# Optimization experiments

Hardware: AMD Instinct MI355X
Metric: run time of the kernel (lower is better)

The kernel has to match this reference:

```python
import jax, jax.numpy as jnp
import numpy as np

L, B, S, D, W = 3, 32, 512, 512, 3
EPS = 1e-6

def setup_inputs() -> dict:
    key = jax.random.key(0)
    ks = jax.random.split(key, 12)
    s = 1.0 / np.sqrt(D)
    def n(k, shape, scale=1.0):
        return jax.random.normal(k, shape, dtype=jnp.float32) * scale
    return {
        'x': n(ks[0], (B, S, D)),
        'fwd_pad': n(ks[1], (L, W, D), s),
        'bwd_pad': n(ks[2], (L, W, D), s),
        'fwd_w': n(ks[3], (L, W + 1)),
        'bwd_w': n(ks[4], (L, W + 1)),
        'fwd_w1': n(ks[5], (L, D, D), s),
        'fwd_b1': jnp.zeros((L, D), jnp.float32),
        'fwd_w2': n(ks[6], (L, D, D), s),
        'fwd_b2': jnp.zeros((L, D), jnp.float32),
        'fwd_g': jnp.ones((L, D), jnp.float32),
        'fwd_beta': jnp.zeros((L, D), jnp.float32),
        'bwd_w1': n(ks[7], (L, D, D), s),
        'bwd_b1': jnp.zeros((L, D), jnp.float32),
        'bwd_w2': n(ks[8], (L, D, D), s),
        'bwd_b2': jnp.zeros((L, D), jnp.float32),
        'bwd_g': jnp.ones((L, D), jnp.float32),
        'bwd_beta': jnp.zeros((L, D), jnp.float32),
    }

def _ln(y, g, b):
    # Annotated-transformer LayerNorm: a2*(x-mean)/(std+eps)+b2, unbiased std
    m = y.mean(-1, keepdims=True)
    sd = jnp.std(y, -1, keepdims=True, ddof=1)
    return g * (y - m) / (sd + EPS) + b

def _ffn(y, w1, b1, w2, b2):
    h = jax.nn.relu(jnp.einsum('bsd,de->bse', y, w1) + b1)
    return jnp.einsum('bse,ef->bsf', h, w2) + b2

def _wsum(padded, w, seq_len, offset):
    # weighted sum over a sliding window of width W+1 (dropout=0, eval mode)
    win = jnp.stack([padded[:, offset + k: offset + k + seq_len] for k in range(W + 1)], 0)
    return jnp.einsum('k,kbsd->bsd', w, win)

def reference(x, fwd_pad, bwd_pad, fwd_w, bwd_w,
              fwd_w1, fwd_b1, fwd_w2, fwd_b2, fwd_g, fwd_beta,
              bwd_w1, bwd_b1, bwd_w2, bwd_b2, bwd_g, bwd_beta):
    bsz, seq_len, _ = x.shape
    xf, xb = x, x
    outs = []
    for i in range(L):
        fp = jnp.broadcast_to(fwd_pad[i], (bsz, W, D))
        bp = jnp.broadcast_to(bwd_pad[i], (bsz, W, D))
        pf = jnp.concatenate([fp, xf, bp], axis=1)  # [B, S+2W, D]
        pb = jnp.concatenate([fp, xb, bp], axis=1)
        yf = _wsum(pf, fwd_w[i], seq_len, 0)       # windows [t, t+W]
        yb = _wsum(pb, bwd_w[i], seq_len, W)       # windows [t+W, t+2W]
        xf = yf + _ffn(_ln(yf, fwd_g[i], fwd_beta[i]), fwd_w1[i], fwd_b1[i], fwd_w2[i], fwd_b2[i])
        xb = yb + _ffn(_ln(yb, bwd_g[i], bwd_beta[i]), bwd_w1[i], bwd_b1[i], bwd_w2[i], bwd_b2[i])
        outs.append(jnp.concatenate([xf, xb], axis=-1))
    return jnp.stack(outs, 0)  # [L, B, S, 2D]
```

## Files before the change

kernel.cpp:

```cpp
#include <hip/hip_runtime.h>

#define S_LEN 512
#define D_DIM 512
#define BATCH 32
#define M_ROWS (BATCH * S_LEN)
#define NLAYER 3

typedef unsigned short ushort_t;
typedef __bf16 bf16_t;
typedef bf16_t bf16x8 __attribute__((ext_vector_type(8)));
typedef unsigned short u16x8 __attribute__((ext_vector_type(8)));
typedef float f32x4 __attribute__((ext_vector_type(4)));

typedef const __attribute__((address_space(1))) unsigned int* gptr_t;
typedef __attribute__((address_space(3))) unsigned int* lptr_t;

__device__ __forceinline__ ushort_t f2bf(float f) {
  unsigned u = __float_as_uint(f);
  unsigned r = (u + 0x7fffu + ((u >> 16) & 1u)) >> 16;
  return (ushort_t)r;
}

__global__ __launch_bounds__(256)
void wprep_kernel(const float* __restrict__ fw1, const float* __restrict__ fw2,
                  const float* __restrict__ bw1, const float* __restrict__ bw2,
                  ushort_t* __restrict__ wt1, ushort_t* __restrict__ wt2) {
  int z = blockIdx.z;
  int l = z >> 2, m = z & 3;
  const float* bases[4] = {fw1, fw2, bw1, bw2};
  const float* src = bases[m] + (size_t)l * D_DIM * D_DIM;
  int streamIdx = m >> 1;
  int which = m & 1;
  ushort_t* dst = (which ? wt2 : wt1) + ((size_t)streamIdx * NLAYER + l) * D_DIM * D_DIM;

  __shared__ float tile[32][33];
  int n0 = blockIdx.x * 32, k0 = blockIdx.y * 32;
  int tx = threadIdx.x, ty = threadIdx.y;
#pragma unroll
  for (int i = 0; i < 32; i += 8)
    tile[ty + i][tx] = src[(size_t)(k0 + ty + i) * D_DIM + n0 + tx];
  __syncthreads();
#pragma unroll
  for (int i = 0; i < 32; i += 8)
    dst[(size_t)(n0 + ty + i) * D_DIM + k0 + tx] = f2bf(tile[tx][ty + i]);
}

__global__ __launch_bounds__(256)
void conv_ln_kernel(const float* __restrict__ srcF, int strideF,
                    const float* __restrict__ srcB, int strideB,
                    const float* __restrict__ padLo, const float* __restrict__ padHi,
                    const float* __restrict__ wF, const float* __restrict__ wB,
                    const float* __restrict__ gF, const float* __restrict__ beF,
                    const float* __restrict__ gB, const float* __restrict__ beB,
                    ushort_t* __restrict__ yln) {
  int z = blockIdx.y;
  int tid = threadIdx.x;
  int lane = tid & 63;
  int rl = tid >> 6;
  int row = blockIdx.x * 4 + rl;
  int t = row & (S_LEN - 1);
  const float* src = z ? srcB : srcF;
  int stride = z ? strideB : strideF;
  const float* wv = z ? wB : wF;
  const float* gv = z ? gB : gF;
  const float* bv = z ? beB : beF;
  int toff = z ? 0 : -3;
  int c0 = lane * 4, c1 = 256 + lane * 4;

  float4 a0 = make_float4(0.f, 0.f, 0.f, 0.f);
  float4 a1 = make_float4(0.f, 0.f, 0.f, 0.f);
#pragma unroll
  for (int k = 0; k < 4; ++k) {
    int tt = t + k + toff;
    const float* rp;
    if (tt < 0)            rp = padLo + (size_t)(tt + 3) * D_DIM;
    else if (tt >= S_LEN)  rp = padHi + (size_t)(tt - S_LEN) * D_DIM;
    else                   rp = src + (size_t)(row + k + toff) * stride;
    float wk = wv[k];
    float4 u0 = *(const float4*)(rp + c0);
    float4 u1 = *(const float4*)(rp + c1);
    a0.x = fmaf(wk, u0.x, a0.x); a0.y = fmaf(wk, u0.y, a0.y);
    a0.z = fmaf(wk, u0.z, a0.z); a0.w = fmaf(wk, u0.w, a0.w);
    a1.x = fmaf(wk, u1.x, a1.x); a1.y = fmaf(wk, u1.y, a1.y);
    a1.z = fmaf(wk, u1.z, a1.z); a1.w = fmaf(wk, u1.w, a1.w);
  }
  float s = a0.x + a0.y + a0.z + a0.w + a1.x + a1.y + a1.z + a1.w;
#pragma unroll
  for (int o = 32; o; o >>= 1) s += __shfl_xor(s, o);
  float mean = s * (1.0f / 512.0f);
  float q = 0.f, dx;
  dx = a0.x - mean; q = fmaf(dx, dx, q);
  dx = a0.y - mean; q = fmaf(dx, dx, q);
  dx = a0.z - mean; q = fmaf(dx, dx, q);
  dx = a0.w - mean; q = fmaf(dx, dx, q);
  dx = a1.x - mean; q = fmaf(dx, dx, q);
  dx = a1.y - mean; q = fmaf(dx, dx, q);
  dx = a1.z - mean; q = fmaf(dx, dx, q);
  dx = a1.w - mean; q = fmaf(dx, dx, q);
#pragma unroll
  for (int o = 32; o; o >>= 1) q += __shfl_xor(q, o);
  float sd = sqrtf(q * (1.0f / 511.0f));
  float inv = 1.0f / (sd + 1e-6f);

  size_t base = ((size_t)z * M_ROWS + row) * D_DIM;
  float4 g0 = *(const float4*)(gv + c0), g1 = *(const float4*)(gv + c1);
  float4 b0 = *(const float4*)(bv + c0), b1 = *(const float4*)(bv + c1);
  ushort_t p0[4], p1[4];
  p0[0] = f2bf(g0.x * ((a0.x - mean) * inv) + b0.x);
  p0[1] = f2bf(g0.y * ((a0.y - mean) * inv) + b0.y);
  p0[2] = f2bf(g0.z * ((a0.z - mean) * inv) + b0.z);
  p0[3] = f2bf(g0.w * ((a0.w - mean) * inv) + b0.w);
  p1[0] = f2bf(g1.x * ((a1.x - mean) * inv) + b1.x);
  p1[1] = f2bf(g1.y * ((a1.y - mean) * inv) + b1.y);
  p1[2] = f2bf(g1.z * ((a1.z - mean) * inv) + b1.z);
  p1[3] = f2bf(g1.w * ((a1.w - mean) * inv) + b1.w);
  *(uint2*)(yln + base + c0) = *(uint2*)p0;
  *(uint2*)(yln + base + c1) = *(uint2*)p1;
}

template <int EPI>
__global__ __launch_bounds__(256)
void gemm_kernel(const ushort_t* __restrict__ A,
                 const ushort_t* __restrict__ Bt_f, const ushort_t* __restrict__ Bt_b,
                 const float* __restrict__ bias_f, const float* __restrict__ bias_b,
                 ushort_t* __restrict__ Hout,
                 float* __restrict__ Cout,
                 const float* __restrict__ srcF, const float* __restrict__ srcB,
                 int srcStride,
                 const float* __restrict__ padLo, const float* __restrict__ padHi,
                 const float* __restrict__ wF, const float* __restrict__ wB) {
  const int K = 512;
  int lin = blockIdx.x;
  int xcd = lin & 7;
  int slot = lin >> 3;
  int nblk = slot & 3;
  int G = xcd * 32 + (slot >> 2);
  int z = G >> 7;
  int mblk = G & 127;

  const ushort_t* Ab = A + (size_t)z * M_ROWS * K + (size_t)mblk * 128 * K;
  const ushort_t* Bb = (z ? Bt_b : Bt_f) + (size_t)nblk * 128 * K;

  __shared__ __attribute__((aligned(16))) ushort_t As[128 * 32];
  __shared__ __attribute__((aligned(16))) ushort_t Bs[128 * 32];

  int tid = threadIdx.x, lane = tid & 63, wave = tid >> 6;
  int wr = wave >> 1, wc = wave & 1;
  int lm = lane & 15, lq = lane >> 4;

  f32x4 acc[4][4] = {};

  for (int kb = 0; kb < 16; ++kb) {
    int k0 = kb * 32;
#pragma unroll
    for (int i = 0; i < 2; ++i) {
      int slot2 = i * 256 + tid;
      int row = slot2 >> 2, kc = slot2 & 3;
      const ushort_t* ga = Ab + (size_t)row * K + k0 + kc * 8;
      const ushort_t* gb = Bb + (size_t)row * K + k0 + kc * 8;
      __builtin_amdgcn_global_load_lds((gptr_t)(const void*)ga,
                                       (lptr_t)(void*)(As + slot2 * 8), 16, 0, 0);
      __builtin_amdgcn_global_load_lds((gptr_t)(const void*)gb,
                                       (lptr_t)(void*)(Bs + slot2 * 8), 16, 0, 0);
    }
    __syncthreads();
    bf16x8 a[4], b[4];
#pragma unroll
    for (int i = 0; i < 4; ++i) {
      union { u16x8 u; bf16x8 b; } ua, ub;
      ua.u = *(const u16x8*)&As[(wr * 64 + i * 16 + lm) * 32 + lq * 8];
      ub.u = *(const u16x8*)&Bs[(wc * 64 + i * 16 + lm) * 32 + lq * 8];
      a[i] = ua.b; b[i] = ub.b;
    }
#pragma unroll
    for (int i = 0; i < 4; ++i)
#pragma unroll
      for (int j = 0; j < 4; ++j)
        acc[i][j] = __builtin_amdgcn_mfma_f32_16x16x32_bf16(a[i], b[j], acc[i][j], 0, 0, 0);
    __syncthreads();
  }

  const float* bias = z ? bias_b : bias_f;
  if (EPI == 1) {
    ushort_t* Hb = Hout + (size_t)z * M_ROWS * 512;
#pragma unroll
    for (int i = 0; i < 4; ++i) {
      int mbase = mblk * 128 + wr * 64 + i * 16 + lq * 4;
#pragma unroll
      for (int j = 0; j < 4; ++j) {
        int n = nblk * 128 + wc * 64 + j * 16 + lm;
        float bvn = bias[n];
#pragma unroll
        for (int r = 0; r < 4; ++r) {
          float v = fmaxf(acc[i][j][r] + bvn, 0.0f);
          Hb[(size_t)(mbase + r) * 512 + n] = f2bf(v);
        }
      }
    }
  } else {
    const float* src = z ? srcB : srcF;
    const float* wv = z ? wB : wF;
    int toff = z ? 0 : -3;
    float w0 = wv[0], w1 = wv[1], w2 = wv[2], w3 = wv[3];
    float* Cb = Cout + (size_t)z * 512;
#pragma unroll
    for (int i = 0; i < 4; ++i) {
      int mbase = mblk * 128 + wr * 64 + i * 16 + lq * 4;
      int t0 = mbase & (S_LEN - 1);
      int rb = mbase - t0;
      const float* rp[7];
#pragma unroll
      for (int q = 0; q < 7; ++q) {
        int tt = t0 + toff + q;
        rp[q] = (tt < 0)       ? padLo + (size_t)(tt + 3) * D_DIM
              : (tt >= S_LEN)  ? padHi + (size_t)(tt - S_LEN) * D_DIM
                               : src + (size_t)(rb + tt) * srcStride;
      }
#pragma unroll
      for (int j = 0; j < 4; ++j) {
        int n = nblk * 128 + wc * 64 + j * 16 + lm;
        float v[7];
#pragma unroll
        for (int q = 0; q < 7; ++q) v[q] = rp[q][n];
        float bvn = bias[n];
#pragma unroll
        for (int r = 0; r < 4; ++r) {
          float y = w0 * v[r] + w1 * v[r + 1] + w2 * v[r + 2] + w3 * v[r + 3];
          Cb[(size_t)(mbase + r) * 1024 + n] = acc[i][j][r] + bvn + y;
        }
      }
    }
  }
}

extern "C" void kernel_launch(void* const* d_in, const int* in_sizes, int n_in,
                              void* d_out, int out_size, void* d_ws, size_t ws_size,
                              hipStream_t stream) {
  const float* x        = (const float*)d_in[0];
  const float* fwd_pad  = (const float*)d_in[1];
  const float* bwd_pad  = (const float*)d_in[2];
  const float* fwd_w    = (const float*)d_in[3];
  const float* bwd_w    = (const float*)d_in[4];
  const float* fwd_w1   = (const float*)d_in[5];
  const float* fwd_b1   = (const float*)d_in[6];
  const float* fwd_w2   = (const float*)d_in[7];
  const float* fwd_b2   = (const float*)d_in[8];
  const float* fwd_g    = (const float*)d_in[9];
  const float* fwd_beta = (const float*)d_in[10];
  const float* bwd_w1   = (const float*)d_in[11];
  const float* bwd_b1   = (const float*)d_in[12];
  const float* bwd_w2   = (const float*)d_in[13];
  const float* bwd_b2   = (const float*)d_in[14];
  const float* bwd_g    = (const float*)d_in[15];
  const float* bwd_beta = (const float*)d_in[16];
  float* out = (float*)d_out;

  const size_t WSZ = (size_t)D_DIM * D_DIM;
  ushort_t* wt1 = (ushort_t*)d_ws;
  ushort_t* wt2 = wt1 + 2 * NLAYER * WSZ;
  ushort_t* yln = wt2 + 2 * NLAYER * WSZ;
  ushort_t* h   = yln + (size_t)2 * M_ROWS * D_DIM;

  wprep_kernel<<<dim3(16, 16, 12), dim3(32, 8), 0, stream>>>(
      fwd_w1, fwd_w2, bwd_w1, bwd_w2, wt1, wt2);

  for (int l = 0; l < NLAYER; ++l) {
    const float *srcF, *srcB;
    int str;
    if (l == 0) {
      srcF = x; srcB = x; str = 512;
    } else {
      srcF = out + (size_t)(l - 1) * M_ROWS * 1024;
      srcB = srcF + 512;
      str = 1024;
    }
    const float* pLo = fwd_pad + (size_t)l * 3 * D_DIM;
    const float* pHi = bwd_pad + (size_t)l * 3 * D_DIM;

    conv_ln_kernel<<<dim3(M_ROWS / 4, 2), 256, 0, stream>>>(
        srcF, str, srcB, str, pLo, pHi,
        fwd_w + l * 4, bwd_w + l * 4,
        fwd_g + l * D_DIM, fwd_beta + l * D_DIM,
        bwd_g + l * D_DIM, bwd_beta + l * D_DIM,
        yln);

    gemm_kernel<1><<<1024, 256, 0, stream>>>(
        yln, wt1 + (size_t)l * WSZ, wt1 + (size_t)(NLAYER + l) * WSZ,
        fwd_b1 + l * D_DIM, bwd_b1 + l * D_DIM,
        h, nullptr,
        nullptr, nullptr, 0, nullptr, nullptr, nullptr, nullptr);

    gemm_kernel<2><<<1024, 256, 0, stream>>>(
        h, wt2 + (size_t)l * WSZ, wt2 + (size_t)(NLAYER + l) * WSZ,
        fwd_b2 + l * D_DIM, bwd_b2 + l * D_DIM,
        nullptr, out + (size_t)l * M_ROWS * 1024,
        srcF, srcB, str, pLo, pHi,
        fwd_w + l * 4, bwd_w + l * 4);
  }
}
```

Baseline: 513.4 us.

## Store bf16 conv output for residual, widen GEMM K-step, stage H stores through LDS

The conv/LN kernel now also writes the windowed-sum result y as bf16 to a workspace buffer. The second GEMM epilogue reads that residual directly instead of recomputing the 4-tap window from 7 fp32 rows. The GEMM main loop loads a 64-wide K slice per barrier pair, halving the number of syncs. The first GEMM epilogue stages the bf16 ReLU output in LDS so it can be written with coalesced 16-byte row stores. The residual is now rounded to bf16, which costs accuracy, and the extra write plus larger LDS footprint may reduce occupancy.

```diff
diff --git a/kernel.cpp b/kernel.cpp
--- a/kernel.cpp
+++ b/kernel.cpp
@@ -19,6 +19,9 @@
   unsigned u = __float_as_uint(f);
   unsigned r = (u + 0x7fffu + ((u >> 16) & 1u)) >> 16;
   return (ushort_t)r;
+}
+__device__ __forceinline__ float bf2f(ushort_t h) {
+  return __uint_as_float(((unsigned)h) << 16);
 }
 
 __global__ __launch_bounds__(256)
@@ -52,7 +55,7 @@
                     const float* __restrict__ wF, const float* __restrict__ wB,
                     const float* __restrict__ gF, const float* __restrict__ beF,
                     const float* __restrict__ gB, const float* __restrict__ beB,
-                    ushort_t* __restrict__ yln) {
+                    ushort_t* __restrict__ yln, ushort_t* __restrict__ yfb) {
   int z = blockIdx.y;
   int tid = threadIdx.x;
   int lane = tid & 63;
@@ -103,6 +106,13 @@
   float inv = 1.0f / (sd + 1e-6f);
 
   size_t base = ((size_t)z * M_ROWS + row) * D_DIM;
+
+  ushort_t f0[4], f1[4];
+  f0[0] = f2bf(a0.x); f0[1] = f2bf(a0.y); f0[2] = f2bf(a0.z); f0[3] = f2bf(a0.w);
+  f1[0] = f2bf(a1.x); f1[1] = f2bf(a1.y); f1[2] = f2bf(a1.z); f1[3] = f2bf(a1.w);
+  *(uint2*)(yfb + base + c0) = *(uint2*)f0;
+  *(uint2*)(yfb + base + c1) = *(uint2*)f1;
+
   float4 g0 = *(const float4*)(gv + c0), g1 = *(const float4*)(gv + c1);
   float4 b0 = *(const float4*)(bv + c0), b1 = *(const float4*)(bv + c1);
   ushort_t p0[4], p1[4];
@@ -118,6 +128,8 @@
   *(uint2*)(yln + base + c1) = *(uint2*)p1;
 }
 
+#define RPITCH 136
+
 template <int EPI>
 __global__ __launch_bounds__(256)
 void gemm_kernel(const ushort_t* __restrict__ A,
@@ -125,10 +137,7 @@
                  const float* __restrict__ bias_f, const float* __restrict__ bias_b,
                  ushort_t* __restrict__ Hout,
                  float* __restrict__ Cout,
-                 const float* __restrict__ srcF, const float* __restrict__ srcB,
-                 int srcStride,
-                 const float* __restrict__ padLo, const float* __restrict__ padHi,
-                 const float* __restrict__ wF, const float* __restrict__ wB) {
+                 const ushort_t* __restrict__ yfb) {
   const int K = 512;
   int lin = blockIdx.x;
   int xcd = lin & 7;
@@ -141,8 +150,9 @@
   const ushort_t* Ab = A + (size_t)z * M_ROWS * K + (size_t)mblk * 128 * K;
   const ushort_t* Bb = (z ? Bt_b : Bt_f) + (size_t)nblk * 128 * K;
 
-  __shared__ __attribute__((aligned(16))) ushort_t As[128 * 32];
-  __shared__ __attribute__((aligned(16))) ushort_t Bs[128 * 32];
+  __shared__ __attribute__((aligned(16))) ushort_t sm[128 * RPITCH];
+  ushort_t* As = sm;
+  ushort_t* Bs = sm + 8192;
 
   int tid = threadIdx.x, lane = tid & 63, wave = tid >> 6;
   int wr = wave >> 1, wc = wave & 1;
@@ -150,39 +160,66 @@
 
   f32x4 acc[4][4] = {};
 
-  for (int kb = 0; kb < 16; ++kb) {
-    int k0 = kb * 32;
-#pragma unroll
-    for (int i = 0; i < 2; ++i) {
-      int slot2 = i * 256 + tid;
-      int row = slot2 >> 2, kc = slot2 & 3;
-      const ushort_t* ga = Ab + (size_t)row * K + k0 + kc * 8;
-      const ushort_t* gb = Bb + (size_t)row * K + k0 + kc * 8;
+  for (int kb = 0; kb < 8; ++kb) {
+    int k0 = kb * 64;
+#pragma unroll
+    for (int i = 0; i < 4; ++i) {
+      int s2 = i * 256 + tid;
+      int half = s2 >> 9;
+      int rem = s2 & 511;
+      int row = rem >> 2, kc = rem & 3;
+      const ushort_t* ga = Ab + (size_t)row * K + k0 + half * 32 + kc * 8;
+      const ushort_t* gb = Bb + (size_t)row * K + k0 + half * 32 + kc * 8;
       __builtin_amdgcn_global_load_lds((gptr_t)(const void*)ga,
-                                       (lptr_t)(void*)(As + slot2 * 8), 16, 0, 0);
+                                       (lptr_t)(void*)(As + s2 * 8), 16, 0, 0);
       __builtin_amdgcn_global_load_lds((gptr_t)(const void*)gb,
-                                       (lptr_t)(void*)(Bs + slot2 * 8), 16, 0, 0);
+                                       (lptr_t)(void*)(Bs + s2 * 8), 16, 0, 0);
     }
     __syncthreads();
-    bf16x8 a[4], b[4];
-#pragma unroll
-    for (int i = 0; i < 4; ++i) {
-      union { u16x8 u; bf16x8 b; } ua, ub;
-      ua.u = *(const u16x8*)&As[(wr * 64 + i * 16 + lm) * 32 + lq * 8];
-      ub.u = *(const u16x8*)&Bs[(wc * 64 + i * 16 + lm) * 32 + lq * 8];
-      a[i] = ua.b; b[i] = ub.b;
-    }
-#pragma unroll
-    for (int i = 0; i < 4; ++i)
-#pragma unroll
-      for (int j = 0; j < 4; ++j)
-        acc[i][j] = __builtin_amdgcn_mfma_f32_16x16x32_bf16(a[i], b[j], acc[i][j], 0, 0, 0);
+#pragma unroll
+    for (int s = 0; s < 2; ++s) {
+      bf16x8 a[4], b[4];
+#pragma unroll
+      for (int i = 0; i < 4; ++i) {
+        union { u16x8 u; bf16x8 b; } ua, ub;
+        ua.u = *(const u16x8*)&As[s * 4096 + (wr * 64 + i * 16 + lm) * 32 + lq * 8];
+        ub.u = *(const u16x8*)&Bs[s * 4096 + (wc * 64 + i * 16 + lm) * 32 + lq * 8];
+        a[i] = ua.b; b[i] = ub.b;
+      }
+#pragma unroll
+      for (int i = 0; i < 4; ++i)
+#pragma unroll
+        for (int j = 0; j < 4; ++j)
+          acc[i][j] = __builtin_amdgcn_mfma_f32_16x16x32_bf16(a[i], b[j], acc[i][j], 0, 0, 0);
+    }
     __syncthreads();
   }
 
   const float* bias = z ? bias_b : bias_f;
   if (EPI == 1) {
-    ushort_t* Hb = Hout + (size_t)z * M_ROWS * 512;
+#pragma unroll
+    for (int i = 0; i < 4; ++i) {
+      int rl0 = wr * 64 + i * 16 + lq * 4;
+#pragma unroll
+      for (int j = 0; j < 4; ++j) {
+        int cl = wc * 64 + j * 16 + lm;
+        float bvn = bias[nblk * 128 + cl];
+#pragma unroll
+        for (int r = 0; r < 4; ++r)
+          sm[(rl0 + r) * RPITCH + cl] = f2bf(fmaxf(acc[i][j][r] + bvn, 0.0f));
+      }
+    }
+    __syncthreads();
+    int row = tid >> 1, half = tid & 1;
+    const ushort_t* rp = sm + row * RPITCH + half * 64;
+    ushort_t* dst = Hout + (size_t)z * M_ROWS * 512 +
+                    (size_t)(mblk * 128 + row) * 512 + nblk * 128 + half * 64;
+#pragma unroll
+    for (int u = 0; u < 8; ++u)
+      *(uint4*)(dst + u * 8) = *(const uint4*)(rp + u * 8);
+  } else {
+    const ushort_t* rs = yfb + (size_t)z * M_ROWS * 512;
+    float* Cb = Cout + (size_t)z * 512;
 #pragma unroll
     for (int i = 0; i < 4; ++i) {
       int mbase = mblk * 128 + wr * 64 + i * 16 + lq * 4;
@@ -192,40 +229,7 @@
         float bvn = bias[n];
 #pragma unroll
         for (int r = 0; r < 4; ++r) {
-          float v = fmaxf(acc[i][j][r] + bvn, 0.0f);
-          Hb[(size_t)(mbase + r) * 512 + n] = f2bf(v);
-        }
-      }
-    }
-  } else {
-    const float* src = z ? srcB : srcF;
-    const float* wv = z ? wB : wF;
-    int toff = z ? 0 : -3;
-    float w0 = wv[0], w1 = wv[1], w2 = wv[2], w3 = wv[3];
-    float* Cb = Cout + (size_t)z * 512;
-#pragma unroll
-    for (int i = 0; i < 4; ++i) {
-      int mbase = mblk * 128 + wr * 64 + i * 16 + lq * 4;
-      int t0 = mbase & (S_LEN - 1);
-      int rb = mbase - t0;
-      const float* rp[7];
-#pragma unroll
-      for (int q = 0; q < 7; ++q) {
-        int tt = t0 + toff + q;
-        rp[q] = (tt < 0)       ? padLo + (size_t)(tt + 3) * D_DIM
-              : (tt >= S_LEN)  ? padHi + (size_t)(tt - S_LEN) * D_DIM
-                               : src + (size_t)(rb + tt) * srcStride;
-      }
-#pragma unroll
-      for (int j = 0; j < 4; ++j) {
-        int n = nblk * 128 + wc * 64 + j * 16 + lm;
-        float v[7];
-#pragma unroll
-        for (int q = 0; q < 7; ++q) v[q] = rp[q][n];
-        float bvn = bias[n];
-#pragma unroll
-        for (int r = 0; r < 4; ++r) {
-          float y = w0 * v[r] + w1 * v[r + 1] + w2 * v[r + 2] + w3 * v[r + 3];
+          float y = bf2f(rs[(size_t)(mbase + r) * 512 + n]);
           Cb[(size_t)(mbase + r) * 1024 + n] = acc[i][j][r] + bvn + y;
         }
       }
@@ -259,7 +263,8 @@
   ushort_t* wt1 = (ushort_t*)d_ws;
   ushort_t* wt2 = wt1 + 2 * NLAYER * WSZ;
   ushort_t* yln = wt2 + 2 * NLAYER * WSZ;
-  ushort_t* h   = yln + (size_t)2 * M_ROWS * D_DIM;
+  ushort_t* yfb = yln + (size_t)2 * M_ROWS * D_DIM;
+  ushort_t* h   = yfb + (size_t)2 * M_ROWS * D_DIM;
 
   wprep_kernel<<<dim3(16, 16, 12), dim3(32, 8), 0, stream>>>(
       fwd_w1, fwd_w2, bwd_w1, bwd_w2, wt1, wt2);
@@ -282,19 +287,16 @@
         fwd_w + l * 4, bwd_w + l * 4,
         fwd_g + l * D_DIM, fwd_beta + l * D_DIM,
         bwd_g + l * D_DIM, bwd_beta + l * D_DIM,
-        yln);
+        yln, yfb);
 
     gemm_kernel<1><<<1024, 256, 0, stream>>>(
         yln, wt1 + (size_t)l * WSZ, wt1 + (size_t)(NLAYER + l) * WSZ,
         fwd_b1 + l * D_DIM, bwd_b1 + l * D_DIM,
-        h, nullptr,
-        nullptr, nullptr, 0, nullptr, nullptr, nullptr, nullptr);
+        h, nullptr, nullptr);
 
     gemm_kernel<2><<<1024, 256, 0, stream>>>(
         h, wt2 + (size_t)l * WSZ, wt2 + (size_t)(NLAYER + l) * WSZ,
         fwd_b2 + l * D_DIM, bwd_b2 + l * D_DIM,
-        nullptr, out + (size_t)l * M_ROWS * 1024,
-        srcF, srcB, str, pLo, pHi,
-        fwd_w + l * 4, bwd_w + l * 4);
+        nullptr, out + (size_t)l * M_ROWS * 1024, yfb);
   }
 }
```

Result: no change. 522.2 us (+1.7%).
